# Performance work log

Hardware: AMD Instinct MI355X
Metric: run time of the kernel (lower is better)

The kernel has to match this reference:

```python
import jax, jax.numpy as jnp
import numpy as np

D_DYN, D_STAT, H, T, B = 3, 3, 256, 365, 1024


def setup_inputs() -> dict:
    key = jax.random.key(0)
    ks = jax.random.split(key, 8)
    C = D_DYN + H
    s = lambda k, shape: jax.random.normal(k, shape, dtype=jnp.float32) * 0.05
    return {
        "x_dyn": jax.random.normal(ks[0], (B, T, D_DYN), dtype=jnp.float32),
        "x_stat": jax.random.normal(ks[1], (B, D_STAT), dtype=jnp.float32),
        "w_i": s(ks[2], (D_STAT, H)), "b_i": jnp.zeros((H,), jnp.float32),
        "w_f": s(ks[3], (C, H)), "b_f": jnp.zeros((H,), jnp.float32),
        "w_g": s(ks[4], (C, H)), "b_g": jnp.zeros((H,), jnp.float32),
        "w_o": s(ks[5], (C, H)), "b_o": jnp.zeros((H,), jnp.float32),
        "w_head": s(ks[6], (H, 1)), "b_head": jnp.zeros((1,), jnp.float32),
    }


def reference(x_dyn, x_stat, w_i, b_i, w_f, b_f, w_g, b_g, w_o, b_o, w_head, b_head):
    # Static input gate (EA-LSTM): i depends only on static features.
    i = jax.nn.sigmoid(x_stat @ w_i + b_i)  # (B, H)

    # Merge the three gate linears into one (C, 3H) matmul per step and
    # split the concat [x_t, h] into x- and h-parts (equivalent to torch.cat).
    W = jnp.concatenate([w_f, w_g, w_o], axis=1)  # (C, 3H)
    Wx, Wh = W[:D_DYN], W[D_DYN:]                 # (D,3H), (H,3H)
    b = jnp.concatenate([b_f, b_g, b_o])          # (3H,)

    def step(carry, x_t):
        h, c = carry
        z = x_t @ Wx + h @ Wh + b                 # (B, 3H)
        f = jax.nn.sigmoid(z[:, :H])
        g = jnp.tanh(z[:, H:2 * H])
        o = jax.nn.sigmoid(z[:, 2 * H:])
        c = f * c + i * g
        h = o * jnp.tanh(c)
        return (h, c), None

    h0 = jnp.zeros((x_dyn.shape[0], H), x_dyn.dtype)
    c0 = jnp.zeros((x_dyn.shape[0], H), x_dyn.dtype)
    (h, _), _ = jax.lax.scan(step, (h0, c0), jnp.swapaxes(x_dyn, 0, 1))
    # Dropout is identity in eval mode.
    return h @ w_head + b_head  # (B, 1)
```

## Files before the change

kernel.cpp:

```cpp
#include <hip/hip_runtime.h>
#include <hip/hip_bf16.h>

#define T_STEPS 365
#define XLEN    (T_STEPS * 3)
#define H_SZ    256
#define ROWS    8
#define NBLK    128
#define NW      8
#define CPW     32

#define SF1     (-1.4426950408889634f)
#define SF2     (-2.8853900817779268f)

typedef __attribute__((ext_vector_type(8))) short bf16x8;
typedef __attribute__((ext_vector_type(4))) short bf16x4;
typedef __attribute__((ext_vector_type(4))) float f32x4;

__device__ __forceinline__ float fast_sigmoid(float x) {
    return __builtin_amdgcn_rcpf(1.0f + __builtin_amdgcn_exp2f(-1.44269504f * x));
}
__device__ __forceinline__ unsigned short f2bf(float x) {
    __hip_bfloat16 b = __float2bfloat16(x);
    return *reinterpret_cast<unsigned short*>(&b);
}
__device__ __forceinline__ float bf2f(unsigned short v) {
    return __uint_as_float(((unsigned)v) << 16);
}
__device__ __forceinline__ bf16x8 expand4(bf16x4 v) {
    bf16x8 r = (bf16x8)0;
    r[0] = v[0]; r[1] = v[1]; r[2] = v[2]; r[3] = v[3];
    return r;
}

__global__ void __launch_bounds__(256)
xstage(const float* __restrict__ x_dyn, unsigned short* __restrict__ xg)
{
    const int rb = blockIdx.x * ROWS;
    for (int idx = threadIdx.x; idx < T_STEPS * ROWS; idx += 256) {
        const int t = idx % T_STEPS, r = idx / T_STEPS;
        const float* s = x_dyn + (size_t)(rb + r) * XLEN + t * 3;
        bf16x4 pk;
        pk[0] = (short)f2bf(s[0]); pk[1] = (short)f2bf(s[1]);
        pk[2] = (short)f2bf(s[2]); pk[3] = (short)0x3F80;
        *(bf16x4*)&xg[((size_t)blockIdx.x * T_STEPS + t) * 32 + r * 4] = pk;
    }
}

__global__ void __launch_bounds__(512, 2)
ealstm_fused(const unsigned short* __restrict__ xg, const float* __restrict__ x_stat,
             const float* __restrict__ w_i, const float* __restrict__ b_i,
             const float* __restrict__ w_f, const float* __restrict__ b_f,
             const float* __restrict__ w_g, const float* __restrict__ b_g,
             const float* __restrict__ w_o, const float* __restrict__ b_o,
             const float* __restrict__ w_head, const float* __restrict__ b_head,
             float* __restrict__ out)
{
    const int tid   = threadIdx.x;
    const int lane  = tid & 63;
    const int wv    = tid >> 6;
    const int m     = lane & 15;
    const int l16   = lane >> 4;
    const int rb    = blockIdx.x * ROWS;
    const int wbase = wv * CPW;
    const int r_eff  = m & 7;
    const int ct_eff = m >> 3;
    const bool hi    = (m >= 8);

    __shared__ unsigned short wo_lds[4 * 8 * 256 * 8];
    __shared__ unsigned short hbuf[2][4096];
    __shared__ float          red[NW][ROWS];

    for (int idx = tid; idx < 4 * 8 * 8 * 256; idx += 512) {
        const int c    = idx & 255;
        const int e    = (idx >> 8) & 7;
        const int kt   = (idx >> 11) & 7;
        const int l16g = idx >> 14;
        wo_lds[((l16g * 8 + kt) * 256 + c) * 8 + e] =
            f2bf(SF1 * w_o[(3 + kt * 32 + l16g * 8 + e) * H_SZ + c]);
    }
    for (int idx = tid; idx < 4096; idx += 512) ((unsigned int*)hbuf)[idx] = 0u;

    const float* wsrc[3] = {w_f, w_g, w_o};
    const float* bsrc[3] = {b_f, b_g, b_o};
    const float  gsf[3]  = {SF1, SF2, SF1};

    bf16x8 wA[8][2][2];
    bf16x8 wXe[2][3];
#pragma unroll
    for (int ct = 0; ct < 2; ++ct) {
        const int c = wbase + ct * 16 + m;
#pragma unroll
        for (int g = 0; g < 2; ++g)
#pragma unroll
            for (int kt = 0; kt < 8; ++kt) {
                bf16x8 a;
#pragma unroll
                for (int e = 0; e < 8; ++e)
                    a[e] = (short)f2bf(gsf[g] * wsrc[g][(3 + kt * 32 + l16 * 8 + e) * H_SZ + c]);
                wA[kt][ct][g] = a;
            }
#pragma unroll
        for (int g = 0; g < 3; ++g) {
            bf16x4 ax = (bf16x4)0;
            if (l16 == 0) {
                ax[0] = (short)f2bf(gsf[g] * wsrc[g][0 * H_SZ + c]);
                ax[1] = (short)f2bf(gsf[g] * wsrc[g][1 * H_SZ + c]);
                ax[2] = (short)f2bf(gsf[g] * wsrc[g][2 * H_SZ + c]);
                ax[3] = (short)f2bf(gsf[g] * bsrc[g][c]);
            }
            wXe[ct][g] = expand4(ax);
        }
    }

    const int c0 = wbase + ct_eff * 16 + l16 * 4;
    float iv[4], cst[4];
    {
        const float xs0 = x_stat[(rb + r_eff) * 3 + 0];
        const float xs1 = x_stat[(rb + r_eff) * 3 + 1];
        const float xs2 = x_stat[(rb + r_eff) * 3 + 2];
#pragma unroll
        for (int q = 0; q < 4; ++q) {
            const int c = c0 + q;
            iv[q] = fast_sigmoid(b_i[c] + xs0 * w_i[c] + xs1 * w_i[H_SZ + c]
                                        + xs2 * w_i[2 * H_SZ + c]);
            cst[q] = 0.0f;
        }
    }

    const int woff = ((c0 >> 5) * 64 + r_eff + 16 * ((c0 & 31) >> 3)) * 8 + (c0 & 7);

    const unsigned short* xrow   = xg + (size_t)blockIdx.x * T_STEPS * 32 + m * 4;
    const bf16x8*         wobase = (const bf16x8*)&wo_lds[((l16 * 8) * 256 + wbase + m) * 8];

    __syncthreads();

    for (int t = 0; t < T_STEPS; ++t) {
        const int cur = t & 1;
        const bf16x8* hp = (const bf16x8*)hbuf[cur] + lane;
        unsigned short* hw = hbuf[cur ^ 1];

        bf16x8 xf = (bf16x8)0;
        if (l16 == 0 && m < 8) {
            const bf16x4 v = *(const bf16x4*)&xrow[(size_t)t * 32];
            xf[0] = v[0]; xf[1] = v[1]; xf[2] = v[2]; xf[3] = v[3];
        }
        bf16x8 hb[8];
#pragma unroll
        for (int kt = 0; kt < 8; ++kt) hb[kt] = hp[kt * 64];
        bf16x8 wor[8][2];
#pragma unroll
        for (int kt = 0; kt < 8; ++kt) {
            wor[kt][0] = wobase[kt * 256];
            wor[kt][1] = wobase[kt * 256 + 16];
        }

        f32x4 acc[2][3];
        {
            const f32x4 z4 = {0.f, 0.f, 0.f, 0.f};
#pragma unroll
            for (int ct = 0; ct < 2; ++ct)
#pragma unroll
                for (int g = 0; g < 3; ++g)
                    acc[ct][g] = __builtin_amdgcn_mfma_f32_16x16x32_bf16(
                        wXe[ct][g], xf, z4, 0, 0, 0);
        }

#pragma unroll
        for (int kt = 0; kt < 8; ++kt) {
            acc[0][0] = __builtin_amdgcn_mfma_f32_16x16x32_bf16(wA[kt][0][0], hb[kt], acc[0][0], 0, 0, 0);
            acc[0][1] = __builtin_amdgcn_mfma_f32_16x16x32_bf16(wA[kt][0][1], hb[kt], acc[0][1], 0, 0, 0);
            acc[0][2] = __builtin_amdgcn_mfma_f32_16x16x32_bf16(wor[kt][0],   hb[kt], acc[0][2], 0, 0, 0);
            acc[1][0] = __builtin_amdgcn_mfma_f32_16x16x32_bf16(wA[kt][1][0], hb[kt], acc[1][0], 0, 0, 0);
            acc[1][1] = __builtin_amdgcn_mfma_f32_16x16x32_bf16(wA[kt][1][1], hb[kt], acc[1][1], 0, 0, 0);
            acc[1][2] = __builtin_amdgcn_mfma_f32_16x16x32_bf16(wor[kt][1],   hb[kt], acc[1][2], 0, 0, 0);
        }

        float zf[4], zg[4], zo[4];
#pragma unroll
        for (int q = 0; q < 4; ++q) {
            const float sf = __shfl_xor(acc[1][0][q], 8);
            const float sg = __shfl_xor(acc[1][1][q], 8);
            const float so = __shfl_xor(acc[1][2][q], 8);
            zf[q] = hi ? sf : acc[0][0][q];
            zg[q] = hi ? sg : acc[0][1][q];
            zo[q] = hi ? so : acc[0][2][q];
        }

        {
            bf16x4 pk;
#pragma unroll
            for (int q = 0; q < 4; ++q) {
                const float Ef = __builtin_amdgcn_exp2f(zf[q]);
                const float Eg = __builtin_amdgcn_exp2f(zg[q]);
                const float Eo = __builtin_amdgcn_exp2f(zo[q]);
                const float u  = 1.0f + Eg;
                const float v  = 1.0f + Ef;
                const float t2 = iv[q] * (2.0f - u);
                const float cq = (cst[q] * u + t2 * v) *
                                 __builtin_amdgcn_rcpf(u * v);
                cst[q] = cq;
                const float Ec = __builtin_amdgcn_exp2f(SF2 * cq);
                const float hq = (1.0f - Ec) *
                                 __builtin_amdgcn_rcpf((1.0f + Eo) * (1.0f + Ec));
                pk[q] = (short)f2bf(hq);
            }
            *(bf16x4*)&hw[woff] = pk;
        }
        __syncthreads();
    }

    float p = 0.0f;
    {
        const unsigned short* hf = hbuf[1];
        const f32x4 wh = *(const f32x4*)&w_head[c0];
        const bf16x4 hv = *(const bf16x4*)&hf[woff];
#pragma unroll
        for (int q = 0; q < 4; ++q) p += bf2f((unsigned short)hv[q]) * wh[q];
    }
    p += __shfl_xor(p, 8);
    p += __shfl_xor(p, 16);
    p += __shfl_xor(p, 32);
    if (lane < ROWS) red[wv][lane] = p;
    __syncthreads();
    if (tid < ROWS) {
        float s = b_head[0];
#pragma unroll
        for (int w = 0; w < NW; ++w) s += red[w][tid];
        out[rb + tid] = s;
    }
}

extern "C" void kernel_launch(void* const* d_in, const int* in_sizes, int n_in,
                              void* d_out, int out_size, void* d_ws, size_t ws_size,
                              hipStream_t stream)
{
    const float* x_dyn  = (const float*)d_in[0];
    const float* x_stat = (const float*)d_in[1];
    const float* w_i    = (const float*)d_in[2];
    const float* b_i    = (const float*)d_in[3];
    const float* w_f    = (const float*)d_in[4];
    const float* b_f    = (const float*)d_in[5];
    const float* w_g    = (const float*)d_in[6];
    const float* b_g    = (const float*)d_in[7];
    const float* w_o    = (const float*)d_in[8];
    const float* b_o    = (const float*)d_in[9];
    const float* w_head = (const float*)d_in[10];
    const float* b_head = (const float*)d_in[11];

    unsigned short* xg = (unsigned short*)d_ws;

    xstage<<<dim3(NBLK), dim3(256), 0, stream>>>(x_dyn, xg);
    ealstm_fused<<<dim3(NBLK), dim3(512), 0, stream>>>(
        xg, x_stat, w_i, b_i, w_f, b_f, w_g, b_g, w_o, b_o,
        w_head, b_head, (float*)d_out);
}
```

Baseline: 526.6 us.

## Halve rows per block to fill more CUs and fold x projection into fp32 FMAs

Each block now handles 4 batch rows instead of 8, so 256 blocks run instead of 128 and more of the GPU's compute units are busy during the sequential recurrence. The input projection is no longer an extra MFMA pass per step with a separate bf16 staging kernel. Each lane instead reads x_dyn directly and adds the x-weight and bias terms with fp32 FMAs after an extra shuffle-based redistribution. The cost is that MFMA tiles are half-filled with padding rows, so the recurrent weight work per row doubles. Each block also still loads the full weights into LDS.

Measured after the change: 524.3 us (median of 2 runs). Within noise of the previous version (-0.4%).

```diff
diff --git a/kernel.cpp b/kernel.cpp
--- a/kernel.cpp
+++ b/kernel.cpp
@@ -4,8 +4,8 @@
 #define T_STEPS 365
 #define XLEN    (T_STEPS * 3)
 #define H_SZ    256
-#define ROWS    8
-#define NBLK    128
+#define ROWS    4
+#define NBLK    256
 #define NW      8
 #define CPW     32
 
@@ -26,28 +26,9 @@
 __device__ __forceinline__ float bf2f(unsigned short v) {
     return __uint_as_float(((unsigned)v) << 16);
 }
-__device__ __forceinline__ bf16x8 expand4(bf16x4 v) {
-    bf16x8 r = (bf16x8)0;
-    r[0] = v[0]; r[1] = v[1]; r[2] = v[2]; r[3] = v[3];
-    return r;
-}
-
-__global__ void __launch_bounds__(256)
-xstage(const float* __restrict__ x_dyn, unsigned short* __restrict__ xg)
-{
-    const int rb = blockIdx.x * ROWS;
-    for (int idx = threadIdx.x; idx < T_STEPS * ROWS; idx += 256) {
-        const int t = idx % T_STEPS, r = idx / T_STEPS;
-        const float* s = x_dyn + (size_t)(rb + r) * XLEN + t * 3;
-        bf16x4 pk;
-        pk[0] = (short)f2bf(s[0]); pk[1] = (short)f2bf(s[1]);
-        pk[2] = (short)f2bf(s[2]); pk[3] = (short)0x3F80;
-        *(bf16x4*)&xg[((size_t)blockIdx.x * T_STEPS + t) * 32 + r * 4] = pk;
-    }
-}
 
 __global__ void __launch_bounds__(512, 2)
-ealstm_fused(const unsigned short* __restrict__ xg, const float* __restrict__ x_stat,
+ealstm_fused(const float* __restrict__ x_dyn, const float* __restrict__ x_stat,
              const float* __restrict__ w_i, const float* __restrict__ b_i,
              const float* __restrict__ w_f, const float* __restrict__ b_f,
              const float* __restrict__ w_g, const float* __restrict__ b_g,
@@ -62,9 +43,10 @@
     const int l16   = lane >> 4;
     const int rb    = blockIdx.x * ROWS;
     const int wbase = wv * CPW;
-    const int r_eff  = m & 7;
+
+    const int r_eff  = m & 3;
     const int ct_eff = m >> 3;
-    const bool hi    = (m >= 8);
+    const int qp     = ((m >> 2) & 1) * 2;
 
     __shared__ unsigned short wo_lds[4 * 8 * 256 * 8];
     __shared__ unsigned short hbuf[2][4096];
@@ -85,7 +67,6 @@
     const float  gsf[3]  = {SF1, SF2, SF1};
 
     bf16x8 wA[8][2][2];
-    bf16x8 wXe[2][3];
 #pragma unroll
     for (int ct = 0; ct < 2; ++ct) {
         const int c = wbase + ct * 16 + m;
@@ -99,38 +80,43 @@
                     a[e] = (short)f2bf(gsf[g] * wsrc[g][(3 + kt * 32 + l16 * 8 + e) * H_SZ + c]);
                 wA[kt][ct][g] = a;
             }
+    }
+
+    const int cw0 = wbase + ct_eff * 16 + l16 * 4 + qp;
+    f32x4 cxw[2][3];
+#pragma unroll
+    for (int e = 0; e < 2; ++e)
 #pragma unroll
         for (int g = 0; g < 3; ++g) {
-            bf16x4 ax = (bf16x4)0;
-            if (l16 == 0) {
-                ax[0] = (short)f2bf(gsf[g] * wsrc[g][0 * H_SZ + c]);
-                ax[1] = (short)f2bf(gsf[g] * wsrc[g][1 * H_SZ + c]);
-                ax[2] = (short)f2bf(gsf[g] * wsrc[g][2 * H_SZ + c]);
-                ax[3] = (short)f2bf(gsf[g] * bsrc[g][c]);
-            }
-            wXe[ct][g] = expand4(ax);
-        }
-    }
-
-    const int c0 = wbase + ct_eff * 16 + l16 * 4;
-    float iv[4], cst[4];
+            const int c = cw0 + e;
+            f32x4 v;
+            v[0] = gsf[g] * wsrc[g][0 * H_SZ + c];
+            v[1] = gsf[g] * wsrc[g][1 * H_SZ + c];
+            v[2] = gsf[g] * wsrc[g][2 * H_SZ + c];
+            v[3] = gsf[g] * bsrc[g][c];
+            cxw[e][g] = v;
+        }
+
+    float iv[2], cst[2];
     {
         const float xs0 = x_stat[(rb + r_eff) * 3 + 0];
         const float xs1 = x_stat[(rb + r_eff) * 3 + 1];
         const float xs2 = x_stat[(rb + r_eff) * 3 + 2];
 #pragma unroll
-        for (int q = 0; q < 4; ++q) {
-            const int c = c0 + q;
-            iv[q] = fast_sigmoid(b_i[c] + xs0 * w_i[c] + xs1 * w_i[H_SZ + c]
+        for (int e = 0; e < 2; ++e) {
+            const int c = cw0 + e;
+            iv[e] = fast_sigmoid(b_i[c] + xs0 * w_i[c] + xs1 * w_i[H_SZ + c]
                                         + xs2 * w_i[2 * H_SZ + c]);
-            cst[q] = 0.0f;
-        }
-    }
-
-    const int woff = ((c0 >> 5) * 64 + r_eff + 16 * ((c0 & 31) >> 3)) * 8 + (c0 & 7);
-
-    const unsigned short* xrow   = xg + (size_t)blockIdx.x * T_STEPS * 32 + m * 4;
-    const bf16x8*         wobase = (const bf16x8*)&wo_lds[((l16 * 8) * 256 + wbase + m) * 8];
+            cst[e] = 0.0f;
+        }
+    }
+
+    const int kw  = cw0 >> 5;
+    const int kp  = cw0 & 31;
+    const int woff = ((kw * 64) + r_eff + 16 * (kp >> 3)) * 8 + (kp & 7);
+
+    const float*  xr     = x_dyn + (size_t)(rb + r_eff) * XLEN;
+    const bf16x8* wobase = (const bf16x8*)&wo_lds[((l16 * 8) * 256 + wbase + m) * 8];
 
     __syncthreads();
 
@@ -139,72 +125,75 @@
         const bf16x8* hp = (const bf16x8*)hbuf[cur] + lane;
         unsigned short* hw = hbuf[cur ^ 1];
 
-        bf16x8 xf = (bf16x8)0;
-        if (l16 == 0 && m < 8) {
-            const bf16x4 v = *(const bf16x4*)&xrow[(size_t)t * 32];
-            xf[0] = v[0]; xf[1] = v[1]; xf[2] = v[2]; xf[3] = v[3];
-        }
-        bf16x8 hb[8];
-#pragma unroll
-        for (int kt = 0; kt < 8; ++kt) hb[kt] = hp[kt * 64];
-        bf16x8 wor[8][2];
-#pragma unroll
-        for (int kt = 0; kt < 8; ++kt) {
-            wor[kt][0] = wobase[kt * 256];
-            wor[kt][1] = wobase[kt * 256 + 16];
-        }
+        const float x0 = xr[t * 3 + 0];
+        const float x1 = xr[t * 3 + 1];
+        const float x2 = xr[t * 3 + 2];
 
         f32x4 acc[2][3];
         {
             const f32x4 z4 = {0.f, 0.f, 0.f, 0.f};
-#pragma unroll
-            for (int ct = 0; ct < 2; ++ct)
-#pragma unroll
-                for (int g = 0; g < 3; ++g)
-                    acc[ct][g] = __builtin_amdgcn_mfma_f32_16x16x32_bf16(
-                        wXe[ct][g], xf, z4, 0, 0, 0);
-        }
-
-#pragma unroll
-        for (int kt = 0; kt < 8; ++kt) {
-            acc[0][0] = __builtin_amdgcn_mfma_f32_16x16x32_bf16(wA[kt][0][0], hb[kt], acc[0][0], 0, 0, 0);
-            acc[0][1] = __builtin_amdgcn_mfma_f32_16x16x32_bf16(wA[kt][0][1], hb[kt], acc[0][1], 0, 0, 0);
-            acc[0][2] = __builtin_amdgcn_mfma_f32_16x16x32_bf16(wor[kt][0],   hb[kt], acc[0][2], 0, 0, 0);
-            acc[1][0] = __builtin_amdgcn_mfma_f32_16x16x32_bf16(wA[kt][1][0], hb[kt], acc[1][0], 0, 0, 0);
-            acc[1][1] = __builtin_amdgcn_mfma_f32_16x16x32_bf16(wA[kt][1][1], hb[kt], acc[1][1], 0, 0, 0);
-            acc[1][2] = __builtin_amdgcn_mfma_f32_16x16x32_bf16(wor[kt][1],   hb[kt], acc[1][2], 0, 0, 0);
-        }
-
-        float zf[4], zg[4], zo[4];
+            const bf16x8 b0  = hp[0];
+            const bf16x8 wo0 = wobase[0];
+            const bf16x8 wo1 = wobase[16];
+            acc[0][0] = __builtin_amdgcn_mfma_f32_16x16x32_bf16(wA[0][0][0], b0, z4, 0, 0, 0);
+            acc[0][1] = __builtin_amdgcn_mfma_f32_16x16x32_bf16(wA[0][0][1], b0, z4, 0, 0, 0);
+            acc[0][2] = __builtin_amdgcn_mfma_f32_16x16x32_bf16(wo0,         b0, z4, 0, 0, 0);
+            acc[1][0] = __builtin_amdgcn_mfma_f32_16x16x32_bf16(wA[0][1][0], b0, z4, 0, 0, 0);
+            acc[1][1] = __builtin_amdgcn_mfma_f32_16x16x32_bf16(wA[0][1][1], b0, z4, 0, 0, 0);
+            acc[1][2] = __builtin_amdgcn_mfma_f32_16x16x32_bf16(wo1,         b0, z4, 0, 0, 0);
+        }
+#pragma unroll
+        for (int kt = 1; kt < 8; ++kt) {
+            const bf16x8 b   = hp[kt * 64];
+            const bf16x8 wo0 = wobase[kt * 256];
+            const bf16x8 wo1 = wobase[kt * 256 + 16];
+            acc[0][0] = __builtin_amdgcn_mfma_f32_16x16x32_bf16(wA[kt][0][0], b, acc[0][0], 0, 0, 0);
+            acc[0][1] = __builtin_amdgcn_mfma_f32_16x16x32_bf16(wA[kt][0][1], b, acc[0][1], 0, 0, 0);
+            acc[0][2] = __builtin_amdgcn_mfma_f32_16x16x32_bf16(wo0,          b, acc[0][2], 0, 0, 0);
+            acc[1][0] = __builtin_amdgcn_mfma_f32_16x16x32_bf16(wA[kt][1][0], b, acc[1][0], 0, 0, 0);
+            acc[1][1] = __builtin_amdgcn_mfma_f32_16x16x32_bf16(wA[kt][1][1], b, acc[1][1], 0, 0, 0);
+            acc[1][2] = __builtin_amdgcn_mfma_f32_16x16x32_bf16(wo1,          b, acc[1][2], 0, 0, 0);
+        }
+
+        float zA[3][4];
 #pragma unroll
         for (int q = 0; q < 4; ++q) {
-            const float sf = __shfl_xor(acc[1][0][q], 8);
-            const float sg = __shfl_xor(acc[1][1][q], 8);
-            const float so = __shfl_xor(acc[1][2][q], 8);
-            zf[q] = hi ? sf : acc[0][0][q];
-            zg[q] = hi ? sg : acc[0][1][q];
-            zo[q] = hi ? so : acc[0][2][q];
-        }
-
+#pragma unroll
+            for (int g = 0; g < 3; ++g) {
+                const float s = __shfl_xor(acc[1][g][q], 8);
+                zA[g][q] = (m >= 8) ? s : acc[0][g][q];
+            }
+        }
+        float z[3][2];
+#pragma unroll
+        for (int g = 0; g < 3; ++g) {
+            const float u2 = __shfl_xor(zA[g][2], 4);
+            const float u3 = __shfl_xor(zA[g][3], 4);
+            z[g][0] = (m & 4) ? u2 : zA[g][0];
+            z[g][1] = (m & 4) ? u3 : zA[g][1];
+        }
+
+        unsigned short h2[2];
+#pragma unroll
+        for (int e = 0; e < 2; ++e) {
+            const float zf = z[0][e] + cxw[e][0][3] + x0 * cxw[e][0][0] + x1 * cxw[e][0][1] + x2 * cxw[e][0][2];
+            const float zg = z[1][e] + cxw[e][1][3] + x0 * cxw[e][1][0] + x1 * cxw[e][1][1] + x2 * cxw[e][1][2];
+            const float zo = z[2][e] + cxw[e][2][3] + x0 * cxw[e][2][0] + x1 * cxw[e][2][1] + x2 * cxw[e][2][2];
+            const float Ef = __builtin_amdgcn_exp2f(zf);
+            const float Eg = __builtin_amdgcn_exp2f(zg);
+            const float Eo = __builtin_amdgcn_exp2f(zo);
+            const float u  = 1.0f + Eg;
+            const float v  = 1.0f + Ef;
+            const float t2 = iv[e] * (2.0f - u);
+            const float cq = (cst[e] * u + t2 * v) * __builtin_amdgcn_rcpf(u * v);
+            cst[e] = cq;
+            const float Ec = __builtin_amdgcn_exp2f(SF2 * cq);
+            const float hq = (1.0f - Ec) * __builtin_amdgcn_rcpf((1.0f + Eo) * (1.0f + Ec));
+            h2[e] = f2bf(hq);
+        }
         {
-            bf16x4 pk;
-#pragma unroll
-            for (int q = 0; q < 4; ++q) {
-                const float Ef = __builtin_amdgcn_exp2f(zf[q]);
-                const float Eg = __builtin_amdgcn_exp2f(zg[q]);
-                const float Eo = __builtin_amdgcn_exp2f(zo[q]);
-                const float u  = 1.0f + Eg;
-                const float v  = 1.0f + Ef;
-                const float t2 = iv[q] * (2.0f - u);
-                const float cq = (cst[q] * u + t2 * v) *
-                                 __builtin_amdgcn_rcpf(u * v);
-                cst[q] = cq;
-                const float Ec = __builtin_amdgcn_exp2f(SF2 * cq);
-                const float hq = (1.0f - Ec) *
-                                 __builtin_amdgcn_rcpf((1.0f + Eo) * (1.0f + Ec));
-                pk[q] = (short)f2bf(hq);
-            }
-            *(bf16x4*)&hw[woff] = pk;
+            unsigned int pk = (unsigned)h2[0] | ((unsigned)h2[1] << 16);
+            *(unsigned int*)&hw[woff] = pk;
         }
         __syncthreads();
     }
@@ -212,11 +201,11 @@
     float p = 0.0f;
     {
         const unsigned short* hf = hbuf[1];
-        const f32x4 wh = *(const f32x4*)&w_head[c0];
-        const bf16x4 hv = *(const bf16x4*)&hf[woff];
-#pragma unroll
-        for (int q = 0; q < 4; ++q) p += bf2f((unsigned short)hv[q]) * wh[q];
-    }
+        const unsigned int hv = *(const unsigned int*)&hf[woff];
+        p = bf2f((unsigned short)(hv & 0xffff)) * w_head[cw0]
+          + bf2f((unsigned short)(hv >> 16))    * w_head[cw0 + 1];
+    }
+    p += __shfl_xor(p, 4);
     p += __shfl_xor(p, 8);
     p += __shfl_xor(p, 16);
     p += __shfl_xor(p, 32);
@@ -247,10 +236,7 @@
     const float* w_head = (const float*)d_in[10];
     const float* b_head = (const float*)d_in[11];
 
-    unsigned short* xg = (unsigned short*)d_ws;
-
-    xstage<<<dim3(NBLK), dim3(256), 0, stream>>>(x_dyn, xg);
     ealstm_fused<<<dim3(NBLK), dim3(512), 0, stream>>>(
-        xg, x_stat, w_i, b_i, w_f, b_f, w_g, b_g, w_o, b_o,
+        x_dyn, x_stat, w_i, b_i, w_f, b_f, w_g, b_g, w_o, b_o,
         w_head, b_head, (float*)d_out);
 }
```
